# Performance work log

Hardware: AMD Instinct MI355X
Metric: run time of the kernel (lower is better)

## Reference

```python
import jax, jax.numpy as jnp
import numpy as np

B, N, I, J = 8, 2048, 64, 32
DA, DB = 64, 16
SCALE = DA ** -0.5


def setup_inputs() -> dict:
    key = jax.random.key(0)
    ks = jax.random.split(key, 9)
    s = lambda fan_in: 1.0 / np.sqrt(fan_in)
    return {
        "voxel_code": jax.random.normal(ks[0], (B, N, I, DA), jnp.float32),
        "trans_code": jax.random.normal(ks[1], (B, N, J, DB), jnp.float32),
        # linear weights stored as (in, out); PyTorch computes x @ W.T, equivalent math
        "Wq": jax.random.uniform(ks[2], (DA, DA), jnp.float32, -s(DA), s(DA)),
        "Wk": jax.random.uniform(ks[3], (DB, DA), jnp.float32, -s(DB), s(DB)),
        "Wv": jax.random.uniform(ks[4], (DB, DA), jnp.float32, -s(DB), s(DB)),
        "Wo": jax.random.uniform(ks[5], (DA, DA), jnp.float32, -s(DA), s(DA)),
        "bo": jax.random.uniform(ks[6], (DA,), jnp.float32, -s(DA), s(DA)),
        "ln_g": jnp.ones((DA,), jnp.float32),
        "ln_b": jnp.zeros((DA,), jnp.float32),
    }


def _layer_norm(x, g, b, eps=1e-5):
    mu = jnp.mean(x, axis=-1, keepdims=True)
    var = jnp.mean(jnp.square(x - mu), axis=-1, keepdims=True)
    return (x - mu) * jax.lax.rsqrt(var + eps) * g + b


def reference(voxel_code, trans_code, Wq, Wk, Wv, Wo, bo, ln_g, ln_b):
    q = jnp.einsum("bnid,de->bnie", voxel_code, Wq)        # [B,N,I,DA]
    k = jnp.einsum("bnjd,de->bnje", trans_code, Wk)        # [B,N,J,DA]
    v = jnp.einsum("bnjd,de->bnje", trans_code, Wv)        # [B,N,J,DA]
    attn = jax.nn.softmax(jnp.einsum("bnie,bnje->bnij", q, k) * SCALE, axis=-1)
    o = jnp.einsum("bnij,bnje->bnie", attn, v) + voxel_code  # residual
    # to_out: Linear -> Dropout(eval: identity) -> LayerNorm(eps=1e-5)
    return _layer_norm(o @ Wo + bo, ln_g, ln_b)
```

## Files before the change

### kernel.cpp

```cpp
#include <hip/hip_runtime.h>
#include <hip/hip_bf16.h>
#include <stdint.h>

typedef __attribute__((ext_vector_type(8))) __bf16 bf16x8;
typedef __attribute__((ext_vector_type(4))) __bf16 bf16x4;
typedef __attribute__((ext_vector_type(4))) float f32x4;
typedef __attribute__((ext_vector_type(4))) unsigned int u32x4;

#define MFMA16(a,b,c) __builtin_amdgcn_mfma_f32_16x16x32_bf16((a),(b),(c),0,0,0)

#define BATCH 8
#define NPTS  2048

__device__ __forceinline__ int swz128(int row, int col) {
    return row*128 + ((col*2) ^ (((row + (row >> 3)) & 7) << 4));
}
__device__ __forceinline__ int swz64(int row, int col) {
    return row*64 + ((col*2) ^ (((row + (row >> 2)) & 3) << 4));
}
__device__ __forceinline__ __bf16* p128(char* base, int row, int col) {
    return (__bf16*)(base + swz128(row, col));
}
__device__ __forceinline__ __bf16* p64(char* base, int row, int col) {
    return (__bf16*)(base + swz64(row, col));
}
__device__ __forceinline__ bf16x8 ld8_128(char* base, int row, int col) {
    return *(const bf16x8*)p128(base, row, col);
}
__device__ __forceinline__ bf16x8 ld8_64(char* base, int row, int col) {
    return *(const bf16x8*)p64(base, row, col);
}

__global__ void prep_weights(const float* __restrict__ Wq, const float* __restrict__ Wk,
                             const float* __restrict__ Wv, const float* __restrict__ Wo,
                             __bf16* __restrict__ ws)
{
    int idx = blockIdx.x * 256 + threadIdx.x;
    char* wsb = (char*)ws;
    if (idx < 4096) {
        int n = idx >> 6, k = idx & 63;
        *(__bf16*)(wsb + swz128(n, k)) = (__bf16)Wo[k*64 + n];
    } else if (idx < 6144) {
        int i = idx - 4096, f = i >> 5, db = i & 31;
        float acc = 0.f;
        if (db < 16) {
            for (int e = 0; e < 64; ++e) acc += Wv[db*64 + e] * Wo[e*64 + f];
        }
        *(__bf16*)(wsb + 8192 + swz64(f, db)) = (__bf16)acc;
    } else if (idx < 7168) {
        int i = idx - 6144, db = i >> 6, d = i & 63;
        float acc = 0.f;
        for (int e = 0; e < 64; ++e) acc += Wq[d*64 + e] * Wk[db*64 + e];
        *(__bf16*)(wsb + 12288 + db*128 + d*2) = (__bf16)(acc * 0.125f);
    }
}

__global__ void __launch_bounds__(256, 6) xattn_kernel(
    const float* __restrict__ voxel, const float* __restrict__ trans,
    const float* __restrict__ ws,
    const float* __restrict__ bo, const float* __restrict__ lng,
    const float* __restrict__ lnb, float* __restrict__ out)
{
    __shared__ __align__(16) char lds[24576];
    char* Wot = lds;
    char* W2t = lds + 8192;
    char* Xb  = lds + 12288;
    char* XPb = lds + 20480;

    const int tid = threadIdx.x;
    const int bn  = blockIdx.x;
    const int w   = tid >> 6;
    const int l   = tid & 63;
    const int l15 = l & 15;
    const int lq  = l >> 4;

    const f32x4 fzero = {0.f, 0.f, 0.f, 0.f};

    bf16x8 mf0, mf1, tfrag[2], ttf;
    {
        const char* wsb = (const char*)ws;
        u32x4 wimg[3];
        #pragma unroll
        for (int i = 0; i < 3; ++i)
            wimg[i] = *(const u32x4*)(wsb + i*4096 + tid*16);
        #pragma unroll
        for (int i = 0; i < 3; ++i)
            *(u32x4*)(lds + i*4096 + tid*16) = wimg[i];
        mf0 = *(const bf16x8*)(wsb + 12288 + l15*128 + lq*16);
        mf1 = *(const bf16x8*)(wsb + 12288 + l15*128 + 64 + lq*16);
        #pragma unroll
        for (int i = 0; i < 8; ++i) { tfrag[0][i] = (__bf16)0.f; tfrag[1][i] = (__bf16)0.f; }
        if (lq < 2) {
            #pragma unroll
            for (int tj = 0; tj < 2; ++tj) {
                const f32x4* gT = (const f32x4*)(trans + (size_t)bn*512 + (16*tj + l15)*16 + lq*8);
                f32x4 u0 = gT[0], u1 = gT[1];
                #pragma unroll
                for (int i = 0; i < 4; ++i) {
                    tfrag[tj][i]     = (__bf16)u0[i];
                    tfrag[tj][i + 4] = (__bf16)u1[i];
                }
            }
        }
        {
            const float* gT = trans + (size_t)bn * 512;
            float tt[8];
            #pragma unroll
            for (int i = 0; i < 8; ++i) tt[i] = gT[(lq*8 + i)*16 + l15];
            #pragma unroll
            for (int i = 0; i < 8; ++i) ttf[i] = (__bf16)tt[i];
        }
        const f32x4* gX = (const f32x4*)(voxel + (size_t)bn * 4096);
        #pragma unroll
        for (int j = 0; j < 4; ++j) {
            f32x4 v = gX[j*256 + tid];
            int gi  = j*256 + tid;
            int row = gi >> 4;
            int col = (gi & 15) * 4;
            bf16x4 h;
            #pragma unroll
            for (int i = 0; i < 4; ++i) h[i] = (__bf16)v[i];
            *(bf16x4*)p128(Xb, row, col) = h;
        }
        if (tid < 128) {
            f32x4 z = {0.f, 0.f, 0.f, 0.f};
            *(f32x4*)p64(XPb, tid >> 1, 16 + (tid & 1)*8) = z;
        }
    }
    asm volatile("s_waitcnt vmcnt(0) lgkmcnt(0)" ::: "memory");
    __syncthreads();

    bf16x8 xa0 = ld8_128(Xb, 16*w + l15, lq*8);
    bf16x8 xa1 = ld8_128(Xb, 16*w + l15, 32 + lq*8);

    {
        f32x4 xm = MFMA16(xa0, mf0, fzero);
        xm = MFMA16(xa1, mf1, xm);
        #pragma unroll
        for (int r = 0; r < 4; ++r)
            *p64(XPb, 16*w + lq*4 + r, l15) = (__bf16)xm[r];
    }
    {
        bf16x8 xma = ld8_64(XPb, 16*w + l15, lq*8);
        f32x4 s0 = MFMA16(xma, tfrag[0], fzero);
        f32x4 s1 = MFMA16(xma, tfrag[1], fzero);
        #pragma unroll
        for (int r = 0; r < 4; ++r) {
            float p0 = __expf(s0[r]);
            float p1 = __expf(s1[r]);
            float su = p0 + p1;
            #pragma unroll
            for (int off = 1; off < 16; off <<= 1) su += __shfl_xor(su, off);
            float inv = __builtin_amdgcn_rcpf(su);
            *p64(XPb, 16*w + lq*4 + r, l15)      = (__bf16)(p0 * inv);
            *p64(XPb, 16*w + lq*4 + r, 16 + l15) = (__bf16)(p1 * inv);
        }
    }
    {
        bf16x8 ap = ld8_64(XPb, 16*w + l15, lq*8);
        f32x4 pt = MFMA16(ap, ttf, fzero);
        #pragma unroll
        for (int r = 0; r < 4; ++r) {
            *p64(XPb, 16*w + lq*4 + r, l15)      = (__bf16)pt[r];
            *p64(XPb, 16*w + lq*4 + r, 16 + l15) = (__bf16)0.f;
        }
    }
    {
        bf16x8 pta = ld8_64(XPb, 16*w + l15, lq*8);
        float bo4[4], g4[4], b4[4];
        #pragma unroll
        for (int t = 0; t < 4; ++t) {
            int c = 16*t + l15;
            bo4[t] = bo[c]; g4[t] = lng[c]; b4[t] = lnb[c];
        }
        f32x4 y[4];
        #pragma unroll
        for (int t = 0; t < 4; ++t) {
            bf16x8 b0  = ld8_128(Wot, 16*t + l15, lq*8);
            bf16x8 b1  = ld8_128(Wot, 16*t + l15, 32 + lq*8);
            bf16x8 w2b = ld8_64 (W2t, 16*t + l15, lq*8);
            y[t] = MFMA16(xa0, b0, fzero);
            y[t] = MFMA16(xa1, b1, y[t]);
            y[t] = MFMA16(pta, w2b, y[t]);
        }
        float* gout = out + (size_t)bn * 4096;
        #pragma unroll
        for (int r = 0; r < 4; ++r) {
            float v0 = y[0][r] + bo4[0];
            float v1 = y[1][r] + bo4[1];
            float v2 = y[2][r] + bo4[2];
            float v3 = y[3][r] + bo4[3];
            float s1 = v0 + v1 + v2 + v3;
            float s2 = v0*v0 + v1*v1 + v2*v2 + v3*v3;
            #pragma unroll
            for (int off = 1; off < 16; off <<= 1) {
                s1 += __shfl_xor(s1, off);
                s2 += __shfl_xor(s2, off);
            }
            float mu  = s1 * 0.015625f;
            float var = s2 * 0.015625f - mu * mu;
            float rs  = rsqrtf(var + 1e-5f);
            int row = 16*w + lq*4 + r;
            gout[row*64 +      l15] = (v0 - mu) * rs * g4[0] + b4[0];
            gout[row*64 + 16 + l15] = (v1 - mu) * rs * g4[1] + b4[1];
            gout[row*64 + 32 + l15] = (v2 - mu) * rs * g4[2] + b4[2];
            gout[row*64 + 48 + l15] = (v3 - mu) * rs * g4[3] + b4[3];
        }
    }
}

extern "C" void kernel_launch(void* const* d_in, const int* in_sizes, int n_in,
                              void* d_out, int out_size, void* d_ws, size_t ws_size,
                              hipStream_t stream) {
    const float* voxel = (const float*)d_in[0];
    const float* trans = (const float*)d_in[1];
    const float* Wq = (const float*)d_in[2];
    const float* Wk = (const float*)d_in[3];
    const float* Wv = (const float*)d_in[4];
    const float* Wo = (const float*)d_in[5];
    const float* bo = (const float*)d_in[6];
    const float* g  = (const float*)d_in[7];
    const float* b  = (const float*)d_in[8];
    float* o = (float*)d_out;

    prep_weights<<<dim3(28), dim3(256), 0, stream>>>(Wq, Wk, Wv, Wo, (__bf16*)d_ws);
    xattn_kernel<<<dim3(BATCH * NPTS), dim3(256), 0, stream>>>(
        voxel, trans, (const float*)d_ws, bo, g, b, o);
}
```

Measured before the change: 130.7 us.

## Make attention kernel persistent and load voxel fragments directly into registers

New measurement: 159.9 us. 22.4% more time.

```diff
diff --git a/kernel.cpp b/kernel.cpp
--- a/kernel.cpp
+++ b/kernel.cpp
@@ -3,7 +3,6 @@
 #include <stdint.h>
 
 typedef __attribute__((ext_vector_type(8))) __bf16 bf16x8;
-typedef __attribute__((ext_vector_type(4))) __bf16 bf16x4;
 typedef __attribute__((ext_vector_type(4))) float f32x4;
 typedef __attribute__((ext_vector_type(4))) unsigned int u32x4;
 
@@ -11,6 +10,8 @@
 
 #define BATCH 8
 #define NPTS  2048
+#define NBN   (BATCH * NPTS)
+#define GRID  1536
 
 __device__ __forceinline__ int swz128(int row, int col) {
     return row*128 + ((col*2) ^ (((row + (row >> 3)) & 7) << 4));
@@ -18,14 +19,11 @@
 __device__ __forceinline__ int swz64(int row, int col) {
     return row*64 + ((col*2) ^ (((row + (row >> 2)) & 3) << 4));
 }
-__device__ __forceinline__ __bf16* p128(char* base, int row, int col) {
-    return (__bf16*)(base + swz128(row, col));
-}
 __device__ __forceinline__ __bf16* p64(char* base, int row, int col) {
     return (__bf16*)(base + swz64(row, col));
 }
 __device__ __forceinline__ bf16x8 ld8_128(char* base, int row, int col) {
-    return *(const bf16x8*)p128(base, row, col);
+    return *(const bf16x8*)(base + swz128(row, col));
 }
 __device__ __forceinline__ bf16x8 ld8_64(char* base, int row, int col) {
     return *(const bf16x8*)p64(base, row, col);
@@ -61,14 +59,12 @@
     const float* __restrict__ bo, const float* __restrict__ lng,
     const float* __restrict__ lnb, float* __restrict__ out)
 {
-    __shared__ __align__(16) char lds[24576];
+    __shared__ __align__(16) char lds[16384];
     char* Wot = lds;
     char* W2t = lds + 8192;
-    char* Xb  = lds + 12288;
-    char* XPb = lds + 20480;
+    char* XPb = lds + 12288;
 
     const int tid = threadIdx.x;
-    const int bn  = blockIdx.x;
     const int w   = tid >> 6;
     const int l   = tid & 63;
     const int l15 = l & 15;
@@ -76,7 +72,8 @@
 
     const f32x4 fzero = {0.f, 0.f, 0.f, 0.f};
 
-    bf16x8 mf0, mf1, tfrag[2], ttf;
+    bf16x8 mf0, mf1;
+    float bo4[4], g4[4], b4[4];
     {
         const char* wsb = (const char*)ws;
         u32x4 wimg[3];
@@ -89,7 +86,38 @@
         mf0 = *(const bf16x8*)(wsb + 12288 + l15*128 + lq*16);
         mf1 = *(const bf16x8*)(wsb + 12288 + l15*128 + 64 + lq*16);
         #pragma unroll
-        for (int i = 0; i < 8; ++i) { tfrag[0][i] = (__bf16)0.f; tfrag[1][i] = (__bf16)0.f; }
+        for (int t = 0; t < 4; ++t) {
+            int c = 16*t + l15;
+            bo4[t] = bo[c]; g4[t] = lng[c]; b4[t] = lnb[c];
+        }
+        if (tid < 128) {
+            f32x4 z = {0.f, 0.f, 0.f, 0.f};
+            *(f32x4*)p64(XPb, tid >> 1, 16 + (tid & 1)*8) = z;
+        }
+    }
+    asm volatile("s_waitcnt vmcnt(0) lgkmcnt(0)" ::: "memory");
+    __syncthreads();
+
+    bf16x8 tfrag[2];
+    #pragma unroll
+    for (int i = 0; i < 8; ++i) { tfrag[0][i] = (__bf16)0.f; tfrag[1][i] = (__bf16)0.f; }
+
+    for (int bn = blockIdx.x; bn < NBN; bn += GRID) {
+        bf16x8 xa0, xa1, ttf;
+        {
+            const f32x4* gXr = (const f32x4*)(voxel + (size_t)bn*4096 + (16*w + l15)*64 + lq*8);
+            f32x4 x0 = gXr[0];
+            f32x4 x1 = gXr[1];
+            f32x4 x2 = gXr[8];
+            f32x4 x3 = gXr[9];
+            #pragma unroll
+            for (int i = 0; i < 4; ++i) {
+                xa0[i]     = (__bf16)x0[i];
+                xa0[i + 4] = (__bf16)x1[i];
+                xa1[i]     = (__bf16)x2[i];
+                xa1[i + 4] = (__bf16)x3[i];
+            }
+        }
         if (lq < 2) {
             #pragma unroll
             for (int tj = 0; tj < 2; ++tj) {
@@ -110,101 +138,74 @@
             #pragma unroll
             for (int i = 0; i < 8; ++i) ttf[i] = (__bf16)tt[i];
         }
-        const f32x4* gX = (const f32x4*)(voxel + (size_t)bn * 4096);
-        #pragma unroll
-        for (int j = 0; j < 4; ++j) {
-            f32x4 v = gX[j*256 + tid];
-            int gi  = j*256 + tid;
-            int row = gi >> 4;
-            int col = (gi & 15) * 4;
-            bf16x4 h;
-            #pragma unroll
-            for (int i = 0; i < 4; ++i) h[i] = (__bf16)v[i];
-            *(bf16x4*)p128(Xb, row, col) = h;
-        }
-        if (tid < 128) {
-            f32x4 z = {0.f, 0.f, 0.f, 0.f};
-            *(f32x4*)p64(XPb, tid >> 1, 16 + (tid & 1)*8) = z;
-        }
-    }
-    asm volatile("s_waitcnt vmcnt(0) lgkmcnt(0)" ::: "memory");
-    __syncthreads();
-
-    bf16x8 xa0 = ld8_128(Xb, 16*w + l15, lq*8);
-    bf16x8 xa1 = ld8_128(Xb, 16*w + l15, 32 + lq*8);
-
-    {
-        f32x4 xm = MFMA16(xa0, mf0, fzero);
-        xm = MFMA16(xa1, mf1, xm);
-        #pragma unroll
-        for (int r = 0; r < 4; ++r)
-            *p64(XPb, 16*w + lq*4 + r, l15) = (__bf16)xm[r];
-    }
-    {
-        bf16x8 xma = ld8_64(XPb, 16*w + l15, lq*8);
-        f32x4 s0 = MFMA16(xma, tfrag[0], fzero);
-        f32x4 s1 = MFMA16(xma, tfrag[1], fzero);
-        #pragma unroll
-        for (int r = 0; r < 4; ++r) {
-            float p0 = __expf(s0[r]);
-            float p1 = __expf(s1[r]);
-            float su = p0 + p1;
-            #pragma unroll
-            for (int off = 1; off < 16; off <<= 1) su += __shfl_xor(su, off);
-            float inv = __builtin_amdgcn_rcpf(su);
-            *p64(XPb, 16*w + lq*4 + r, l15)      = (__bf16)(p0 * inv);
-            *p64(XPb, 16*w + lq*4 + r, 16 + l15) = (__bf16)(p1 * inv);
-        }
-    }
-    {
-        bf16x8 ap = ld8_64(XPb, 16*w + l15, lq*8);
-        f32x4 pt = MFMA16(ap, ttf, fzero);
-        #pragma unroll
-        for (int r = 0; r < 4; ++r) {
-            *p64(XPb, 16*w + lq*4 + r, l15)      = (__bf16)pt[r];
-            *p64(XPb, 16*w + lq*4 + r, 16 + l15) = (__bf16)0.f;
-        }
-    }
-    {
-        bf16x8 pta = ld8_64(XPb, 16*w + l15, lq*8);
-        float bo4[4], g4[4], b4[4];
-        #pragma unroll
-        for (int t = 0; t < 4; ++t) {
-            int c = 16*t + l15;
-            bo4[t] = bo[c]; g4[t] = lng[c]; b4[t] = lnb[c];
-        }
-        f32x4 y[4];
-        #pragma unroll
-        for (int t = 0; t < 4; ++t) {
-            bf16x8 b0  = ld8_128(Wot, 16*t + l15, lq*8);
-            bf16x8 b1  = ld8_128(Wot, 16*t + l15, 32 + lq*8);
-            bf16x8 w2b = ld8_64 (W2t, 16*t + l15, lq*8);
-            y[t] = MFMA16(xa0, b0, fzero);
-            y[t] = MFMA16(xa1, b1, y[t]);
-            y[t] = MFMA16(pta, w2b, y[t]);
-        }
-        float* gout = out + (size_t)bn * 4096;
-        #pragma unroll
-        for (int r = 0; r < 4; ++r) {
-            float v0 = y[0][r] + bo4[0];
-            float v1 = y[1][r] + bo4[1];
-            float v2 = y[2][r] + bo4[2];
-            float v3 = y[3][r] + bo4[3];
-            float s1 = v0 + v1 + v2 + v3;
-            float s2 = v0*v0 + v1*v1 + v2*v2 + v3*v3;
-            #pragma unroll
-            for (int off = 1; off < 16; off <<= 1) {
-                s1 += __shfl_xor(s1, off);
-                s2 += __shfl_xor(s2, off);
-            }
-            float mu  = s1 * 0.015625f;
-            float var = s2 * 0.015625f - mu * mu;
-            float rs  = rsqrtf(var + 1e-5f);
-            int row = 16*w + lq*4 + r;
-            gout[row*64 +      l15] = (v0 - mu) * rs * g4[0] + b4[0];
-            gout[row*64 + 16 + l15] = (v1 - mu) * rs * g4[1] + b4[1];
-            gout[row*64 + 32 + l15] = (v2 - mu) * rs * g4[2] + b4[2];
-            gout[row*64 + 48 + l15] = (v3 - mu) * rs * g4[3] + b4[3];
+
+        {
+            f32x4 xm = MFMA16(xa0, mf0, fzero);
+            xm = MFMA16(xa1, mf1, xm);
+            #pragma unroll
+            for (int r = 0; r < 4; ++r)
+                *p64(XPb, 16*w + lq*4 + r, l15) = (__bf16)xm[r];
+        }
+        {
+            bf16x8 xma = ld8_64(XPb, 16*w + l15, lq*8);
+            f32x4 s0 = MFMA16(xma, tfrag[0], fzero);
+            f32x4 s1 = MFMA16(xma, tfrag[1], fzero);
+            #pragma unroll
+            for (int r = 0; r < 4; ++r) {
+                float p0 = __expf(s0[r]);
+                float p1 = __expf(s1[r]);
+                float su = p0 + p1;
+                #pragma unroll
+                for (int off = 1; off < 16; off <<= 1) su += __shfl_xor(su, off);
+                float inv = __builtin_amdgcn_rcpf(su);
+                *p64(XPb, 16*w + lq*4 + r, l15)      = (__bf16)(p0 * inv);
+                *p64(XPb, 16*w + lq*4 + r, 16 + l15) = (__bf16)(p1 * inv);
+            }
+        }
+        {
+            bf16x8 ap = ld8_64(XPb, 16*w + l15, lq*8);
+            f32x4 pt = MFMA16(ap, ttf, fzero);
+            #pragma unroll
+            for (int r = 0; r < 4; ++r) {
+                *p64(XPb, 16*w + lq*4 + r, l15)      = (__bf16)pt[r];
+                *p64(XPb, 16*w + lq*4 + r, 16 + l15) = (__bf16)0.f;
+            }
+        }
+        {
+            bf16x8 pta = ld8_64(XPb, 16*w + l15, lq*8);
+            f32x4 y[4];
+            #pragma unroll
+            for (int t = 0; t < 4; ++t) {
+                bf16x8 b0  = ld8_128(Wot, 16*t + l15, lq*8);
+                bf16x8 b1  = ld8_128(Wot, 16*t + l15, 32 + lq*8);
+                bf16x8 w2b = ld8_64 (W2t, 16*t + l15, lq*8);
+                y[t] = MFMA16(xa0, b0, fzero);
+                y[t] = MFMA16(xa1, b1, y[t]);
+                y[t] = MFMA16(pta, w2b, y[t]);
+            }
+            float* gout = out + (size_t)bn * 4096;
+            #pragma unroll
+            for (int r = 0; r < 4; ++r) {
+                float v0 = y[0][r] + bo4[0];
+                float v1 = y[1][r] + bo4[1];
+                float v2 = y[2][r] + bo4[2];
+                float v3 = y[3][r] + bo4[3];
+                float s1 = v0 + v1 + v2 + v3;
+                float s2 = v0*v0 + v1*v1 + v2*v2 + v3*v3;
+                #pragma unroll
+                for (int off = 1; off < 16; off <<= 1) {
+                    s1 += __shfl_xor(s1, off);
+                    s2 += __shfl_xor(s2, off);
+                }
+                float mu  = s1 * 0.015625f;
+                float var = s2 * 0.015625f - mu * mu;
+                float rs  = rsqrtf(var + 1e-5f);
+                int row = 16*w + lq*4 + r;
+                gout[row*64 +      l15] = (v0 - mu) * rs * g4[0] + b4[0];
+                gout[row*64 + 16 + l15] = (v1 - mu) * rs * g4[1] + b4[1];
+                gout[row*64 + 32 + l15] = (v2 - mu) * rs * g4[2] + b4[2];
+                gout[row*64 + 48 + l15] = (v3 - mu) * rs * g4[3] + b4[3];
+            }
         }
     }
 }
@@ -224,6 +225,6 @@
     float* o = (float*)d_out;
 
     prep_weights<<<dim3(28), dim3(256), 0, stream>>>(Wq, Wk, Wv, Wo, (__bf16*)d_ws);
-    xattn_kernel<<<dim3(BATCH * NPTS), dim3(256), 0, stream>>>(
+    xattn_kernel<<<dim3(GRID), dim3(256), 0, stream>>>(
         voxel, trans, (const float*)d_ws, bo, g, b, o);
 }
```
